# Kernel optimization log

Hardware: AMD Instinct MI355X
Metric: run time of the kernel (lower is better)

## Reference

```python
import jax, jax.numpy as jnp
import numpy as np
from jax import lax

DIM = 1024
DIM_INNER = 2048  # int(dim * expansion_factor)


def log_g(x):
    # log-space g(x): where(x>=0, log(relu(x)+0.5), -softplus(-x))
    return jnp.where(x >= 0, jnp.log(jax.nn.relu(x) + 0.5), -jax.nn.softplus(-x))


def heinsen_associative_scan_log(log_coeffs, log_values):
    # parallel log-space linear recurrence over the sequence axis (axis=1)
    a_star = jnp.cumsum(log_coeffs, axis=1)
    log_h0_plus_b_star = lax.cumlogsumexp(log_values - a_star, axis=1)
    return a_star + log_h0_plus_b_star


def setup_inputs() -> dict:
    key = jax.random.key(0)
    k_x, k_w1, k_w2 = jax.random.split(key, 3)
    x = jax.random.normal(k_x, (4, 4096, DIM), dtype=jnp.float32)
    # Linear(dim, 2*dim_inner, bias=False): store as [in, out] for x @ W
    W_hg = jax.random.normal(k_w1, (DIM, 2 * DIM_INNER), dtype=jnp.float32) * (1.0 / np.sqrt(DIM))
    W_out = jax.random.normal(k_w2, (DIM_INNER, DIM), dtype=jnp.float32) * (1.0 / np.sqrt(DIM_INNER))
    return {"x": x, "W_hg": W_hg, "W_out": W_out}


def reference(x, W_hg, W_out):
    # x: [b, s, dim]
    hg = jnp.einsum('bsd,de->bse', x, W_hg)  # [b, s, 2*dim_inner]
    hidden, gate = jnp.split(hg, 2, axis=-1)
    log_coeffs = -jax.nn.softplus(gate)        # log(1 - z)
    log_z = -jax.nn.softplus(-gate)            # log z
    log_values = log_z + log_g(hidden)
    log_h = heinsen_associative_scan_log(log_coeffs, log_values)  # [b, s, dim_inner]
    out = jnp.exp(log_h)
    return jnp.einsum('bse,ed->bsd', out, W_out)
```

## Files before the change

kernel.cpp:

```cpp
#include <hip/hip_runtime.h>
#include <cmath>

#define DIM 1024
#define DIM_INNER 2048
#define BATCH 4
#define SEQ 4096
#define MTOT (BATCH * SEQ)
#define CHUNK 32
#define NCHUNK (SEQ / CHUNK)

typedef __bf16 bf16x8 __attribute__((ext_vector_type(8)));
typedef short short8_t __attribute__((ext_vector_type(8)));
typedef float floatx4 __attribute__((ext_vector_type(4)));
typedef unsigned short u16x4 __attribute__((ext_vector_type(4)));
typedef unsigned int uint4_t __attribute__((ext_vector_type(4)));
typedef float float4_t __attribute__((ext_vector_type(4)));
typedef unsigned short ushort_t;

template <int N> struct IC { static constexpr int v = N; };
template <bool B> struct BC { static constexpr bool v = B; };

#define LGKM_SB(n) do { asm volatile("s_waitcnt lgkmcnt(" #n ")" ::: "memory"); \
                        __builtin_amdgcn_sched_barrier(0); } while (0)
#define SCHED0() __builtin_amdgcn_sched_barrier(0)
#define SBAR() __builtin_amdgcn_s_barrier()

__device__ __forceinline__ unsigned short f2bf(float f) {
  unsigned int u = __builtin_bit_cast(unsigned int, f);
  u += 0x7fffu + ((u >> 16) & 1u);
  return (unsigned short)(u >> 16);
}
__device__ __forceinline__ float bflo2f(unsigned int u) {
  return __builtin_bit_cast(float, u << 16);
}
__device__ __forceinline__ float bfhi2f(unsigned int u) {
  return __builtin_bit_cast(float, u & 0xffff0000u);
}

__device__ __forceinline__ void lclv_fast(float h, float g, float& lc, float& lv) {
  float eg = __expf(-fabsf(g));
  float sp = fmaxf(g, 0.f) + __logf(1.f + eg);
  lc = -sp;
  float eh = __expf(h);
  float t  = (h >= 0.f) ? (h + 0.5f) : (1.f + eh);
  float lt = __logf(t);
  float lg = (h >= 0.f) ? lt : (h - lt);
  lv = g + lc + lg;
}
__device__ __forceinline__ float logaddexp_f(float a, float b) {
  float m = fmaxf(a, b);
  return m + __logf(1.f + __expf(-fabsf(a - b)));
}

__device__ __forceinline__ void async_copy16(const ushort_t* g, ushort_t* l) {
  __builtin_amdgcn_global_load_lds(
      (const __attribute__((address_space(1))) void*)g,
      (__attribute__((address_space(3))) void*)l, 16, 0, 0);
}

__global__ __launch_bounds__(256) void convert_f32_bf16(
    const float* __restrict__ src, ushort_t* __restrict__ dst) {
  int i = blockIdx.x * 256 + threadIdx.x;
  float4 v = ((const float4*)src)[i];
  u16x4 o = {f2bf(v.x), f2bf(v.y), f2bf(v.z), f2bf(v.w)};
  ((u16x4*)dst)[i] = o;
}

__global__ __launch_bounds__(256) void transpose_f32_bf16(
    const float* __restrict__ src, ushort_t* __restrict__ dst, int K, int N) {
  __shared__ float tile[32][33];
  int tx = threadIdx.x & 31, ty = threadIdx.x >> 5;
  int n0 = blockIdx.x * 32, k0 = blockIdx.y * 32;
#pragma unroll
  for (int i = 0; i < 4; i++) {
    int k = ty + i * 8;
    tile[k][tx] = src[(size_t)(k0 + k) * N + n0 + tx];
  }
  __syncthreads();
#pragma unroll
  for (int i = 0; i < 4; i++) {
    int r = ty + i * 8;
    dst[(size_t)(n0 + r) * K + k0 + tx] = f2bf(tile[tx][r]);
  }
}

#define G1_NT (DIM / 64)
#define G2_NT (DIM_INNER / 64)

__global__ __launch_bounds__(512, 2) void gemm1_fused(
    const ushort_t* __restrict__ Xbf, const ushort_t* __restrict__ Wt,
    unsigned int* __restrict__ LCLV) {
  __shared__ __align__(16) ushort_t lds[81920];

  const int tid = threadIdx.x;
  const int wv = tid >> 6;
  const int lane = tid & 63;
  const int wr = wv >> 2;
  const int wc = wv & 3;
  const int l15 = lane & 15;
  const int quad = lane >> 4;
  const int n0 = blockIdx.x * 128;
  const int m0 = blockIdx.y * 256;

  int aSrc[2][2], bSrc[2][2];
  int dstE[2];
#pragma unroll
  for (int L = 0; L < 2; L++) {
    int e = L * 512 + tid;
    int row = e >> 3, slot = e & 7;
    int sw = (slot ^ (row & 7)) << 3;
    dstE[L] = e * 8;
#pragma unroll
    for (int half = 0; half < 2; half++) {
      aSrc[half][L] = (m0 + half * 128 + row) * DIM + sw;
      int br = half * 128 + row;
      int grow = n0 + ((br >> 6) << 5) + (br & 31) + ((br & 32) ? DIM_INNER : 0);
      bSrc[half][L] = grow * DIM + sw;
    }
  }

  auto stageA = [&](int kt, int half, int buf) {
#pragma unroll
    for (int L = 0; L < 2; L++)
      async_copy16(Xbf + aSrc[half][L] + kt * 64,
                   lds + buf * 16384 + half * 8192 + dstE[L]);
  };
  auto stageB = [&](int kt, int half, int buf) {
#pragma unroll
    for (int L = 0; L < 2; L++)
      async_copy16(Wt + bSrc[half][L] + kt * 64,
                   lds + 49152 + buf * 16384 + half * 8192 + dstE[L]);
  };

  const int swz0 = ((quad ^ (l15 & 7)) << 3);
  const int swz1 = (((4 | quad) ^ (l15 & 7)) << 3);
  const int aB0 = wr * 8192 + l15 * 64 + swz0;
  const int aB1 = wr * 8192 + l15 * 64 + swz1;
  const int bB0 = wc * 4096 + l15 * 64 + swz0;
  const int bB1 = wc * 4096 + l15 * 64 + swz1;

  auto readA = [&](int buf, int mf, int ks) -> bf16x8 {
    const ushort_t* p = lds + buf * 16384 + (ks ? aB1 : aB0) + mf * 1024;
    return __builtin_bit_cast(bf16x8, *(const short8_t*)p);
  };
  auto readB = [&](int buf, int nf, int ks) -> bf16x8 {
    const ushort_t* p = lds + 49152 + buf * 16384 + (ks ? bB1 : bB0) + nf * 1024;
    return __builtin_bit_cast(bf16x8, *(const short8_t*)p);
  };

  floatx4 acc[8][4];
#pragma unroll
  for (int i = 0; i < 8; i++)
#pragma unroll
    for (int j = 0; j < 4; j++) acc[i][j] = (floatx4){0.f, 0.f, 0.f, 0.f};

  bf16x8 aF[4][2], b0F[2][2], b1F[2][2];

  auto mma4 = [&](auto MA, auto MC, auto J, bf16x8 (&bX)[2][2]) {
#pragma unroll
    for (int jj = 0; jj < 2; jj++)
#pragma unroll
      for (int ks = 0; ks < 2; ks++)
        acc[MC.v][J.v + jj] = __builtin_amdgcn_mfma_f32_16x16x32_bf16(
            aF[MA.v][ks], bX[jj][ks], acc[MC.v][J.v + jj], 0, 0, 0);
  };
  auto mmaRow = [&](auto J, bf16x8 (&bvec)[2]) {
#pragma unroll
    for (int m = 0; m < 4; m++)
#pragma unroll
      for (int ks = 0; ks < 2; ks++)
        acc[m][J.v] = __builtin_amdgcn_mfma_f32_16x16x32_bf16(
            aF[m][ks], bvec[ks], acc[m][J.v], 0, 0, 0);
  };

  int bufA = 0, bufB = 0, bufAn = 2, bufBn = 1;

  auto tileBody = [&](int kb, int ka, auto STB, auto STA, auto VMALL) {
    aF[0][0] = readA(bufA, 0, 0); aF[0][1] = readA(bufA, 0, 1);
    b0F[0][0] = readB(bufB, 0, 0); b0F[0][1] = readB(bufB, 0, 1);
    b0F[1][0] = readB(bufB, 1, 0); b0F[1][1] = readB(bufB, 1, 1);
    SCHED0();
    aF[1][0] = readA(bufA, 1, 0); aF[1][1] = readA(bufA, 1, 1);
    SCHED0();
    aF[2][0] = readA(bufA, 2, 0); aF[2][1] = readA(bufA, 2, 1);
    SCHED0();
    aF[3][0] = readA(bufA, 3, 0); aF[3][1] = readA(bufA, 3, 1);
    SCHED0();
    if constexpr (STB.v) stageB(kb, 0, bufBn);
    SBAR();
    __builtin_amdgcn_s_setprio(1);
    LGKM_SB(6); mma4(IC<0>{}, IC<0>{}, IC<0>{}, b0F);
    LGKM_SB(4); mma4(IC<1>{}, IC<1>{}, IC<0>{}, b0F);
    LGKM_SB(2); mma4(IC<2>{}, IC<2>{}, IC<0>{}, b0F);
    LGKM_SB(0); mma4(IC<3>{}, IC<3>{}, IC<0>{}, b0F);
    __builtin_amdgcn_s_setprio(0);
    SBAR();

    b1F[0][0] = readB(bufB, 2, 0); b1F[0][1] = readB(bufB, 2, 1);
    SCHED0();
    b1F[1][0] = readB(bufB, 3, 0); b1F[1][1] = readB(bufB, 3, 1);
    SCHED0();
    if constexpr (STB.v) stageB(kb, 1, bufBn);
    SBAR();
    __builtin_amdgcn_s_setprio(1);
    LGKM_SB(2); mmaRow(IC<2>{}, b1F[0]);
    LGKM_SB(0); mmaRow(IC<3>{}, b1F[1]);
    __builtin_amdgcn_s_setprio(0);
    SBAR();

    aF[0][0] = readA(bufA, 4, 0); aF[0][1] = readA(bufA, 4, 1);
    SCHED0();
    aF[1][0] = readA(bufA, 5, 0); aF[1][1] = readA(bufA, 5, 1);
    SCHED0();
    aF[2][0] = readA(bufA, 6, 0); aF[2][1] = readA(bufA, 6, 1);
    SCHED0();
    aF[3][0] = readA(bufA, 7, 0); aF[3][1] = readA(bufA, 7, 1);
    SCHED0();
    if constexpr (STA.v) stageA(ka, 0, bufAn);
    SBAR();
    __builtin_amdgcn_s_setprio(1);
    LGKM_SB(6); mma4(IC<0>{}, IC<4>{}, IC<2>{}, b1F);
    LGKM_SB(4); mma4(IC<1>{}, IC<5>{}, IC<2>{}, b1F);
    LGKM_SB(2); mma4(IC<2>{}, IC<6>{}, IC<2>{}, b1F);
    LGKM_SB(0); mma4(IC<3>{}, IC<7>{}, IC<2>{}, b1F);
    __builtin_amdgcn_s_setprio(0);
    SBAR();

    if constexpr (STA.v) stageA(ka, 1, bufAn);
    SCHED0();
    if constexpr (STA.v) {
      asm volatile("s_waitcnt vmcnt(4)" ::: "memory");
    } else if constexpr (VMALL.v) {
      asm volatile("s_waitcnt vmcnt(0)" ::: "memory");
    }
    SBAR();
    __builtin_amdgcn_s_setprio(1);
    mma4(IC<0>{}, IC<4>{}, IC<0>{}, b0F);
    mma4(IC<1>{}, IC<5>{}, IC<0>{}, b0F);
    mma4(IC<2>{}, IC<6>{}, IC<0>{}, b0F);
    mma4(IC<3>{}, IC<7>{}, IC<0>{}, b0F);
    __builtin_amdgcn_s_setprio(0);
    SBAR();
  };

  stageB(0, 0, 0); stageB(0, 1, 0);
  stageA(0, 0, 0); stageA(0, 1, 0);
  stageA(1, 0, 1); stageA(1, 1, 1);
  asm volatile("s_waitcnt vmcnt(4)" ::: "memory");
  SBAR();

  for (int u = 0; u < G1_NT - 2; u++) {
    tileBody(u + 1, u + 2, BC<true>{}, BC<true>{}, BC<false>{});
    bufA = (bufA == 2) ? 0 : bufA + 1;
    bufAn = (bufAn == 2) ? 0 : bufAn + 1;
    bufB ^= 1; bufBn ^= 1;
  }
  tileBody(G1_NT - 1, 0, BC<true>{}, BC<false>{}, BC<true>{});
  bufA = (bufA == 2) ? 0 : bufA + 1;
  bufB ^= 1;
  tileBody(0, 0, BC<false>{}, BC<false>{}, BC<false>{});

#pragma unroll
  for (int mf = 0; mf < 8; mf++)
#pragma unroll
    for (int j = 0; j < 2; j++) {
      int col = n0 + wc * 32 + j * 16 + l15;
#pragma unroll
      for (int r = 0; r < 4; r++) {
        int row = m0 + wr * 128 + mf * 16 + quad * 4 + r;
        float lc, lv;
        lclv_fast(acc[mf][j][r], acc[mf][j + 2][r], lc, lv);
        unsigned int pk = ((unsigned int)f2bf(lv) << 16) | (unsigned int)f2bf(lc);
        LCLV[(size_t)row * DIM_INNER + col] = pk;
      }
    }
}

__global__ __launch_bounds__(512, 2) void gemm2(
    const ushort_t* __restrict__ Hbf, const ushort_t* __restrict__ Wot,
    float* __restrict__ OUT) {
  __shared__ __align__(16) ushort_t lds[81920];

  const int tid = threadIdx.x;
  const int wv = tid >> 6;
  const int lane = tid & 63;
  const int wr = wv >> 2;
  const int wc = wv & 3;
  const int l15 = lane & 15;
  const int quad = lane >> 4;
  const int n0 = blockIdx.x * 256;
  const int m0 = blockIdx.y * 256;

  int aSrc[2][2], bSrc[2][2];
  int dstE[2];
#pragma unroll
  for (int L = 0; L < 2; L++) {
    int e = L * 512 + tid;
    int row = e >> 3, slot = e & 7;
    int sw = (slot ^ (row & 7)) << 3;
    dstE[L] = e * 8;
#pragma unroll
    for (int half = 0; half < 2; half++) {
      aSrc[half][L] = (m0 + half * 128 + row) * DIM_INNER + sw;
      bSrc[half][L] = (n0 + half * 128 + row) * DIM_INNER + sw;
    }
  }

  auto stageA = [&](int kt, int half, int buf) {
#pragma unroll
    for (int L = 0; L < 2; L++)
      async_copy16(Hbf + aSrc[half][L] + kt * 64,
                   lds + buf * 16384 + half * 8192 + dstE[L]);
  };
  auto stageB = [&](int kt, int half, int buf) {
#pragma unroll
    for (int L = 0; L < 2; L++)
      async_copy16(Wot + bSrc[half][L] + kt * 64,
                   lds + 49152 + buf * 16384 + half * 8192 + dstE[L]);
  };

  const int swz0 = ((quad ^ (l15 & 7)) << 3);
  const int swz1 = (((4 | quad) ^ (l15 & 7)) << 3);
  const int aB0 = wr * 8192 + l15 * 64 + swz0;
  const int aB1 = wr * 8192 + l15 * 64 + swz1;
  const int bB0 = wc * 4096 + l15 * 64 + swz0;
  const int bB1 = wc * 4096 + l15 * 64 + swz1;

  auto readA = [&](int buf, int mf, int ks) -> bf16x8 {
    const ushort_t* p = lds + buf * 16384 + (ks ? aB1 : aB0) + mf * 1024;
    return __builtin_bit_cast(bf16x8, *(const short8_t*)p);
  };
  auto readB = [&](int buf, int nf, int ks) -> bf16x8 {
    const ushort_t* p = lds + 49152 + buf * 16384 + (ks ? bB1 : bB0) + nf * 1024;
    return __builtin_bit_cast(bf16x8, *(const short8_t*)p);
  };

  floatx4 acc[8][4];
#pragma unroll
  for (int i = 0; i < 8; i++)
#pragma unroll
    for (int j = 0; j < 4; j++) acc[i][j] = (floatx4){0.f, 0.f, 0.f, 0.f};

  bf16x8 aF[4][2], b0F[2][2], b1F[2][2];

  auto mma4 = [&](auto MA, auto MC, auto J, bf16x8 (&bX)[2][2]) {
#pragma unroll
    for (int jj = 0; jj < 2; jj++)
#pragma unroll
      for (int ks = 0; ks < 2; ks++)
        acc[MC.v][J.v + jj] = __builtin_amdgcn_mfma_f32_16x16x32_bf16(
            aF[MA.v][ks], bX[jj][ks], acc[MC.v][J.v + jj], 0, 0, 0);
  };
  auto mmaRow = [&](auto J, bf16x8 (&bvec)[2]) {
#pragma unroll
    for (int m = 0; m < 4; m++)
#pragma unroll
      for (int ks = 0; ks < 2; ks++)
        acc[m][J.v] = __builtin_amdgcn_mfma_f32_16x16x32_bf16(
            aF[m][ks], bvec[ks], acc[m][J.v], 0, 0, 0);
  };

  int bufA = 0, bufB = 0, bufAn = 2, bufBn = 1;

  auto tileBody = [&](int kb, int ka, auto STB, auto STA, auto VMALL) {
    aF[0][0] = readA(bufA, 0, 0); aF[0][1] = readA(bufA, 0, 1);
    b0F[0][0] = readB(bufB, 0, 0); b0F[0][1] = readB(bufB, 0, 1);
    b0F[1][0] = readB(bufB, 1, 0); b0F[1][1] = readB(bufB, 1, 1);
    SCHED0();
    aF[1][0] = readA(bufA, 1, 0); aF[1][1] = readA(bufA, 1, 1);
    SCHED0();
    aF[2][0] = readA(bufA, 2, 0); aF[2][1] = readA(bufA, 2, 1);
    SCHED0();
    aF[3][0] = readA(bufA, 3, 0); aF[3][1] = readA(bufA, 3, 1);
    SCHED0();
    if constexpr (STB.v) stageB(kb, 0, bufBn);
    SBAR();
    __builtin_amdgcn_s_setprio(1);
    LGKM_SB(6); mma4(IC<0>{}, IC<0>{}, IC<0>{}, b0F);
    LGKM_SB(4); mma4(IC<1>{}, IC<1>{}, IC<0>{}, b0F);
    LGKM_SB(2); mma4(IC<2>{}, IC<2>{}, IC<0>{}, b0F);
    LGKM_SB(0); mma4(IC<3>{}, IC<3>{}, IC<0>{}, b0F);
    __builtin_amdgcn_s_setprio(0);
    SBAR();

    b1F[0][0] = readB(bufB, 2, 0); b1F[0][1] = readB(bufB, 2, 1);
    SCHED0();
    b1F[1][0] = readB(bufB, 3, 0); b1F[1][1] = readB(bufB, 3, 1);
    SCHED0();
    if constexpr (STB.v) stageB(kb, 1, bufBn);
    SBAR();
    __builtin_amdgcn_s_setprio(1);
    LGKM_SB(2); mmaRow(IC<2>{}, b1F[0]);
    LGKM_SB(0); mmaRow(IC<3>{}, b1F[1]);
    __builtin_amdgcn_s_setprio(0);
    SBAR();

    aF[0][0] = readA(bufA, 4, 0); aF[0][1] = readA(bufA, 4, 1);
    SCHED0();
    aF[1][0] = readA(bufA, 5, 0); aF[1][1] = readA(bufA, 5, 1);
    SCHED0();
    aF[2][0] = readA(bufA, 6, 0); aF[2][1] = readA(bufA, 6, 1);
    SCHED0();
    aF[3][0] = readA(bufA, 7, 0); aF[3][1] = readA(bufA, 7, 1);
    SCHED0();
    if constexpr (STA.v) stageA(ka, 0, bufAn);
    SBAR();
    __builtin_amdgcn_s_setprio(1);
    LGKM_SB(6); mma4(IC<0>{}, IC<4>{}, IC<2>{}, b1F);
    LGKM_SB(4); mma4(IC<1>{}, IC<5>{}, IC<2>{}, b1F);
    LGKM_SB(2); mma4(IC<2>{}, IC<6>{}, IC<2>{}, b1F);
    LGKM_SB(0); mma4(IC<3>{}, IC<7>{}, IC<2>{}, b1F);
    __builtin_amdgcn_s_setprio(0);
    SBAR();

    if constexpr (STA.v) stageA(ka, 1, bufAn);
    SCHED0();
    if constexpr (STA.v) {
      asm volatile("s_waitcnt vmcnt(4)" ::: "memory");
    } else if constexpr (VMALL.v) {
      asm volatile("s_waitcnt vmcnt(0)" ::: "memory");
    }
    SBAR();
    __builtin_amdgcn_s_setprio(1);
    mma4(IC<0>{}, IC<4>{}, IC<0>{}, b0F);
    mma4(IC<1>{}, IC<5>{}, IC<0>{}, b0F);
    mma4(IC<2>{}, IC<6>{}, IC<0>{}, b0F);
    mma4(IC<3>{}, IC<7>{}, IC<0>{}, b0F);
    __builtin_amdgcn_s_setprio(0);
    SBAR();
  };

  stageB(0, 0, 0); stageB(0, 1, 0);
  stageA(0, 0, 0); stageA(0, 1, 0);
  stageA(1, 0, 1); stageA(1, 1, 1);
  asm volatile("s_waitcnt vmcnt(4)" ::: "memory");
  SBAR();

  for (int u = 0; u < G2_NT - 2; u++) {
    tileBody(u + 1, u + 2, BC<true>{}, BC<true>{}, BC<false>{});
    bufA = (bufA == 2) ? 0 : bufA + 1;
    bufAn = (bufAn == 2) ? 0 : bufAn + 1;
    bufB ^= 1; bufBn ^= 1;
  }
  tileBody(G2_NT - 1, 0, BC<true>{}, BC<false>{}, BC<true>{});
  bufA = (bufA == 2) ? 0 : bufA + 1;
  bufB ^= 1;
  tileBody(0, 0, BC<false>{}, BC<false>{}, BC<false>{});

#pragma unroll
  for (int mf = 0; mf < 8; mf++)
#pragma unroll
    for (int j = 0; j < 4; j++) {
      int col = n0 + wc * 64 + (j >> 1) * 32 + (j & 1) * 16 + l15;
#pragma unroll
      for (int r = 0; r < 4; r++) {
        int row = m0 + wr * 128 + mf * 16 + quad * 4 + r;
        OUT[(size_t)row * DIM + col] = acc[mf][j][r];
      }
    }
}

__global__ __launch_bounds__(256) void scan_phase1(
    const unsigned int* __restrict__ LCLV,
    float* __restrict__ Asum, float* __restrict__ Lend, int nbch) {
  const int EQ = DIM_INNER / 4;
  int tid = blockIdx.x * 256 + threadIdx.x;
  int ep = tid % EQ;
  int tmp = tid / EQ;
  int c = tmp % NCHUNK;
  int bz = tmp / NCHUNK;
  size_t base4 = ((size_t)bz * SEQ + (size_t)c * CHUNK) * EQ + ep;
  const uint4_t* L4 = (const uint4_t*)LCLV;

  float4_t asum = {0.f, 0.f, 0.f, 0.f};
  float4_t logh = {-INFINITY, -INFINITY, -INFINITY, -INFINITY};
#pragma unroll 4
  for (int t = 0; t < CHUNK; t++) {
    uint4_t u = L4[base4 + (size_t)t * EQ];
#pragma unroll
    for (int k = 0; k < 4; k++) {
      float lc = bflo2f(u[k]), lv = bfhi2f(u[k]);
      asum[k] += lc;
      logh[k] = logaddexp_f(lc + logh[k], lv);
    }
  }
  size_t sidx = ((size_t)c * nbch + (size_t)bz * DIM_INNER) / 4 + ep;
  ((float4_t*)Asum)[sidx] = asum;
  ((float4_t*)Lend)[sidx] = logh;
}

__global__ __launch_bounds__(256) void scan_phase2(
    float* Asum, const float* __restrict__ Lend, int nbch) {
  int ch = blockIdx.x * 256 + threadIdx.x;
  float p = -INFINITY;
  for (int c = 0; c < NCHUNK; c++) {
    float a = Asum[(size_t)c * nbch + ch];
    float le = Lend[(size_t)c * nbch + ch];
    Asum[(size_t)c * nbch + ch] = p;
    p = logaddexp_f(a + p, le);
  }
}

__global__ __launch_bounds__(256) void scan_phase3(
    const unsigned int* __restrict__ LCLV, const float* __restrict__ P,
    ushort_t* __restrict__ H, int nbch) {
  const int EQ = DIM_INNER / 4;
  int tid = blockIdx.x * 256 + threadIdx.x;
  int ep = tid % EQ;
  int tmp = tid / EQ;
  int c = tmp % NCHUNK;
  int bz = tmp / NCHUNK;
  size_t base4 = ((size_t)bz * SEQ + (size_t)c * CHUNK) * EQ + ep;
  const uint4_t* L4 = (const uint4_t*)LCLV;
  u16x4* H4 = (u16x4*)H;

  size_t pidx = ((size_t)c * nbch + (size_t)bz * DIM_INNER) / 4 + ep;
  float4_t logh = ((const float4_t*)P)[pidx];
#pragma unroll 4
  for (int t = 0; t < CHUNK; t++) {
    uint4_t u = L4[base4 + (size_t)t * EQ];
    u16x4 hv;
#pragma unroll
    for (int k = 0; k < 4; k++) {
      float lc = bflo2f(u[k]), lv = bfhi2f(u[k]);
      logh[k] = logaddexp_f(lc + logh[k], lv);
      hv[k] = f2bf(__expf(logh[k]));
    }
    H4[base4 + (size_t)t * EQ] = hv;
  }
}

extern "C" void kernel_launch(void* const* d_in, const int* in_sizes, int n_in,
                              void* d_out, int out_size, void* d_ws, size_t ws_size,
                              hipStream_t stream) {
  const float* X = (const float*)d_in[0];
  const float* Whg = (const float*)d_in[1];
  const float* Wout = (const float*)d_in[2];
  float* out = (float*)d_out;

  ushort_t* Xbf = (ushort_t*)d_ws;
  ushort_t* Whg_t = Xbf + (size_t)MTOT * DIM;
  ushort_t* Wout_t = Whg_t + (size_t)(2 * DIM_INNER) * DIM;
  char* pp = (char*)(Wout_t + (size_t)DIM * DIM_INNER);

  const size_t fixed_bytes = (size_t)MTOT * DIM * 2 +
                             (size_t)2 * DIM_INNER * DIM * 2 +
                             (size_t)DIM * DIM_INNER * 2;
  const size_t per_batch = (size_t)SEQ * DIM_INNER * 4 +
                           (size_t)SEQ * DIM_INNER * 2 +
                           2 * (size_t)DIM_INNER * NCHUNK * 4;
  int nb = 4;
  while (nb > 1 && fixed_bytes + (size_t)nb * per_batch > ws_size) nb >>= 1;
  const int npass = BATCH / nb;

  convert_f32_bf16<<<(MTOT * DIM / 4) / 256, 256, 0, stream>>>(X, Xbf);
  transpose_f32_bf16<<<dim3(2 * DIM_INNER / 32, DIM / 32), 256, 0, stream>>>(
      Whg, Whg_t, DIM, 2 * DIM_INNER);
  transpose_f32_bf16<<<dim3(DIM / 32, DIM_INNER / 32), 256, 0, stream>>>(
      Wout, Wout_t, DIM_INNER, DIM);

  for (int pass = 0; pass < npass; pass++) {
    const int b0 = pass * nb;
    const int nrows = nb * SEQ;
    const int nbch = nb * DIM_INNER;

    unsigned int* LCLV = (unsigned int*)pp;
    ushort_t* Hbf = (ushort_t*)(LCLV + (size_t)nb * SEQ * DIM_INNER);
    float* Asum = (float*)(Hbf + (size_t)nb * SEQ * DIM_INNER);
    float* Lend = Asum + (size_t)nb * DIM_INNER * NCHUNK;

    gemm1_fused<<<dim3(DIM_INNER / 128, nrows / 256), 512, 0, stream>>>(
        Xbf + (size_t)b0 * SEQ * DIM, Whg_t, LCLV);
    scan_phase1<<<(nbch / 4 * NCHUNK) / 256, 256, 0, stream>>>(LCLV, Asum, Lend, nbch);
    scan_phase2<<<nbch / 256, 256, 0, stream>>>(Asum, Lend, nbch);
    scan_phase3<<<(nbch / 4 * NCHUNK) / 256, 256, 0, stream>>>(LCLV, Asum, Hbf, nbch);
    gemm2<<<dim3(DIM / 256, nrows / 256), 512, 0, stream>>>(
        Hbf, Wout_t, out + (size_t)b0 * SEQ * DIM);
  }
}
```

Measured before the change: 425.1 us.

## Fuse chunk-level scan reduction into gemm1 epilogue and remap workgroup order

The per-chunk sum of log-coefficients and chunk-end log-sum-exp (scan phase 1) are now computed inside the gemm1 epilogue from the bf16-rounded values it already holds in registers. Lanes combine their partials with cross-lane shuffles, and the two 16-row halves are merged to form 32-row chunks. This removes a kernel launch and a full re-read of the LCLV buffer. Workgroup IDs are also remapped so consecutive blocks are spread across XCD-sized groups, aiming at better cache locality. The cost is a heavier epilogue, with more register pressure and transcendental work in the GEMM.

```diff
diff --git a/kernel.cpp b/kernel.cpp
--- a/kernel.cpp
+++ b/kernel.cpp
@@ -89,7 +89,8 @@
 
 __global__ __launch_bounds__(512, 2) void gemm1_fused(
     const ushort_t* __restrict__ Xbf, const ushort_t* __restrict__ Wt,
-    unsigned int* __restrict__ LCLV) {
+    unsigned int* __restrict__ LCLV,
+    float* __restrict__ Asum, float* __restrict__ Lend, int nbch) {
   __shared__ __align__(16) ushort_t lds[81920];
 
   const int tid = threadIdx.x;
@@ -99,8 +100,13 @@
   const int wc = wv & 3;
   const int l15 = lane & 15;
   const int quad = lane >> 4;
-  const int n0 = blockIdx.x * 128;
-  const int m0 = blockIdx.y * 256;
+
+  const int nwg = gridDim.x * gridDim.y;
+  const int lin = blockIdx.y * gridDim.x + blockIdx.x;
+  const int qchunk = nwg >> 3;
+  const int wid = (lin & 7) * qchunk + (lin >> 3);
+  const int n0 = (wid & 15) * 128;
+  const int m0 = (wid >> 4) * 256;
 
   int aSrc[2][2], bSrc[2][2];
   int dstE[2];
@@ -261,19 +267,54 @@
   tileBody(0, 0, BC<false>{}, BC<false>{}, BC<false>{});
 
 #pragma unroll
-  for (int mf = 0; mf < 8; mf++)
+  for (int c2 = 0; c2 < 4; c2++) {
+    float hA[2][2], hL[2][2];
+#pragma unroll
+    for (int mh = 0; mh < 2; mh++) {
+      int mf = c2 * 2 + mh;
+#pragma unroll
+      for (int j = 0; j < 2; j++) {
+        int col = n0 + wc * 32 + j * 16 + l15;
+        float sA = 0.f, sL = -INFINITY;
+#pragma unroll
+        for (int r = 0; r < 4; r++) {
+          int row = m0 + wr * 128 + mf * 16 + quad * 4 + r;
+          float lc, lv;
+          lclv_fast(acc[mf][j][r], acc[mf][j + 2][r], lc, lv);
+          unsigned int pk = ((unsigned int)f2bf(lv) << 16) | (unsigned int)f2bf(lc);
+          LCLV[(size_t)row * DIM_INNER + col] = pk;
+          float lcr = bflo2f(pk), lvr = bfhi2f(pk);
+          sL = logaddexp_f(sL + lcr, lvr);
+          sA += lcr;
+        }
+        float A = sA, L = sL;
+#pragma unroll
+        for (int st = 16; st <= 32; st <<= 1) {
+          float Ao = __shfl_xor(A, st, 64);
+          float Lo = __shfl_xor(L, st, 64);
+          bool upper = (lane & st) != 0;
+          L = upper ? logaddexp_f(Lo + A, L) : logaddexp_f(L + Ao, Lo);
+          A = A + Ao;
+        }
+        hA[mh][j] = A;
+        hL[mh][j] = L;
+      }
+    }
 #pragma unroll
     for (int j = 0; j < 2; j++) {
-      int col = n0 + wc * 32 + j * 16 + l15;
-#pragma unroll
-      for (int r = 0; r < 4; r++) {
-        int row = m0 + wr * 128 + mf * 16 + quad * 4 + r;
-        float lc, lv;
-        lclv_fast(acc[mf][j][r], acc[mf][j + 2][r], lc, lv);
-        unsigned int pk = ((unsigned int)f2bf(lv) << 16) | (unsigned int)f2bf(lc);
-        LCLV[(size_t)row * DIM_INNER + col] = pk;
+      float A = hA[0][j] + hA[1][j];
+      float L = logaddexp_f(hL[0][j] + hA[1][j], hL[1][j]);
+      if (quad == 0) {
+        int cg = (m0 + wr * 128 + c2 * 32) >> 5;
+        int bz = cg >> 7;
+        int cs = cg & (NCHUNK - 1);
+        int col = n0 + wc * 32 + j * 16 + l15;
+        size_t sidx = (size_t)cs * nbch + (size_t)bz * DIM_INNER + col;
+        Asum[sidx] = A;
+        Lend[sidx] = L;
       }
     }
+  }
 }
 
 __global__ __launch_bounds__(512, 2) void gemm2(
@@ -460,34 +501,6 @@
     }
 }
 
-__global__ __launch_bounds__(256) void scan_phase1(
-    const unsigned int* __restrict__ LCLV,
-    float* __restrict__ Asum, float* __restrict__ Lend, int nbch) {
-  const int EQ = DIM_INNER / 4;
-  int tid = blockIdx.x * 256 + threadIdx.x;
-  int ep = tid % EQ;
-  int tmp = tid / EQ;
-  int c = tmp % NCHUNK;
-  int bz = tmp / NCHUNK;
-  size_t base4 = ((size_t)bz * SEQ + (size_t)c * CHUNK) * EQ + ep;
-  const uint4_t* L4 = (const uint4_t*)LCLV;
-
-  float4_t asum = {0.f, 0.f, 0.f, 0.f};
-  float4_t logh = {-INFINITY, -INFINITY, -INFINITY, -INFINITY};
-#pragma unroll 4
-  for (int t = 0; t < CHUNK; t++) {
-    uint4_t u = L4[base4 + (size_t)t * EQ];
-#pragma unroll
-    for (int k = 0; k < 4; k++) {
-      float lc = bflo2f(u[k]), lv = bfhi2f(u[k]);
-      asum[k] += lc;
-      logh[k] = logaddexp_f(lc + logh[k], lv);
-    }
-  }
-  size_t sidx = ((size_t)c * nbch + (size_t)bz * DIM_INNER) / 4 + ep;
-  ((float4_t*)Asum)[sidx] = asum;
-  ((float4_t*)Lend)[sidx] = logh;
-}
 
 __global__ __launch_bounds__(256) void scan_phase2(
     float* Asum, const float* __restrict__ Lend, int nbch) {
@@ -570,8 +583,7 @@
     float* Lend = Asum + (size_t)nb * DIM_INNER * NCHUNK;
 
     gemm1_fused<<<dim3(DIM_INNER / 128, nrows / 256), 512, 0, stream>>>(
-        Xbf + (size_t)b0 * SEQ * DIM, Whg_t, LCLV);
-    scan_phase1<<<(nbch / 4 * NCHUNK) / 256, 256, 0, stream>>>(LCLV, Asum, Lend, nbch);
+        Xbf + (size_t)b0 * SEQ * DIM, Whg_t, LCLV, Asum, Lend, nbch);
     scan_phase2<<<nbch / 256, 256, 0, stream>>>(Asum, Lend, nbch);
     scan_phase3<<<(nbch / 4 * NCHUNK) / 256, 256, 0, stream>>>(LCLV, Asum, Hbf, nbch);
     gemm2<<<dim3(DIM / 256, nrows / 256), 512, 0, stream>>>(
```

After: 451.8 us. +6.3%, slower.
